# Performance work log

Measured on AMD Instinct MI355X. Metric: run time of the kernel, lower is better.

Reference implementation:

```python
import jax, jax.numpy as jnp
import numpy as np

N_NODES = 100000
N_EDGES = 1600000
N_GRAPHS = 64
IN_F = 128
H_F = 128
N_CLS = 10


def setup_inputs() -> dict:
    key = jax.random.key(0)
    ks = jax.random.split(key, 10)
    feat = jax.random.normal(ks[0], (N_NODES, IN_F), dtype=jnp.float32)
    W1 = jax.random.normal(ks[1], (IN_F, H_F), dtype=jnp.float32) * 0.05
    b1 = jax.random.normal(ks[2], (H_F,), dtype=jnp.float32) * 0.05
    W2 = jax.random.normal(ks[3], (H_F, H_F), dtype=jnp.float32) * 0.05
    b2 = jax.random.normal(ks[4], (H_F,), dtype=jnp.float32) * 0.05
    Wp = jax.random.normal(ks[5], (H_F, N_CLS), dtype=jnp.float32) * 0.05
    bp = jax.random.normal(ks[6], (N_CLS,), dtype=jnp.float32) * 0.05
    src = jax.random.randint(ks[7], (N_EDGES,), 0, N_NODES, dtype=jnp.int32)
    dst = jax.random.randint(ks[8], (N_EDGES,), 0, N_NODES, dtype=jnp.int32)
    graph_id = jnp.sort(jax.random.randint(ks[9], (N_NODES,), 0, N_GRAPHS, dtype=jnp.int32))
    return {"feat": feat, "W1": W1, "b1": b1, "W2": W2, "b2": b2,
            "Wp": Wp, "bp": bp, "src": src, "dst": dst, "graph_id": graph_id}


def reference(feat, W1, b1, W2, b2, Wp, bp, src, dst, graph_id):
    # copy_u + sum: each dst node sums features of its source neighbors
    def agg(h):
        return jax.ops.segment_sum(h[src], dst, num_segments=N_NODES)

    h = jax.nn.relu(agg(feat) @ W1 + b1)   # conv1 + ReLU
    h = jax.nn.relu(agg(h) @ W2 + b2)      # conv2 + ReLU (num_messagepasses=2)

    # dgl.mean_nodes: per-graph mean pooling over nodes
    sums = jax.ops.segment_sum(h, graph_id, num_segments=N_GRAPHS)      # [G, H]
    cnts = jax.ops.segment_sum(jnp.ones((N_NODES, 1), h.dtype), graph_id,
                               num_segments=N_GRAPHS)                    # [G, 1]
    graph_feats = sums / jnp.maximum(cnts, 1.0)
    return graph_feats @ Wp + bp
```

## Files before the change

kernel.cpp:

```cpp
#include <hip/hip_runtime.h>

#define NF 128
#define NGRAPHS 64
#define NCLS 10
#define NPARTS 64
#define PART_SHIFT 11
#define PART_NODES 2048
#define PART_CAP 36864
#define SPLIT_TILE 8192
#define AS_STRIDE 136

typedef __attribute__((ext_vector_type(8))) short bf16x8;
typedef __attribute__((ext_vector_type(4))) float f32x4;
typedef __attribute__((ext_vector_type(8))) unsigned short u16x8;

__device__ __forceinline__ float bf2f(unsigned short u) {
    union { unsigned int i; float f; } v; v.i = ((unsigned int)u) << 16; return v.f;
}
__device__ __forceinline__ unsigned short f2bf(float f) {
    union { float f; unsigned int i; } v; v.f = f;
    unsigned int lsb = (v.i >> 16) & 1;
    v.i += 0x7fffu + lsb;
    return (unsigned short)(v.i >> 16);
}

__global__ __launch_bounds__(256) void prep_all(
    const float* __restrict__ feat, unsigned short* __restrict__ featbf,
    const float* __restrict__ W1, const float* __restrict__ W2,
    unsigned short* __restrict__ Wt1, unsigned short* __restrict__ Wt2,
    float* __restrict__ sums, int* __restrict__ gcur, int nv4) {
    int i = blockIdx.x * blockDim.x + threadIdx.x;
    if (i < nv4) {
        float4 v = ((const float4*)feat)[i];
        ushort4 o;
        o.x = f2bf(v.x); o.y = f2bf(v.y); o.z = f2bf(v.z); o.w = f2bf(v.w);
        ((ushort4*)featbf)[i] = o;
    }
    if (i < 2 * NF * NF) {
        const float* W = (i < NF * NF) ? W1 : W2;
        unsigned short* Wt = (i < NF * NF) ? Wt1 : Wt2;
        int id = i & (NF * NF - 1);
        int f = id >> 7;
        int k = id & 127;
        Wt[f * NF + k] = f2bf(W[k * NF + f]);
    }
    if (i < NGRAPHS * NF) sums[i] = 0.f;
    if (i < NPARTS) gcur[i] = 0;
}

__global__ __launch_bounds__(256) void split_kernel(
    const int* __restrict__ src, const int* __restrict__ dst,
    int2* __restrict__ records, int* __restrict__ gcur, int ne) {
    __shared__ int2 stage[SPLIT_TILE];
    __shared__ int hcnt[NPARTS];
    __shared__ int hbase[NPARTS];
    __shared__ int hcur[NPARTS];
    __shared__ int hg[NPARTS];
    int t = threadIdx.x;
    int tile0 = blockIdx.x * SPLIT_TILE;
    int cnt = min(SPLIT_TILE, ne - tile0);
    if (cnt <= 0) return;
    if (t < NPARTS) hcnt[t] = 0;
    __syncthreads();
    for (int i = t; i < cnt; i += 256) {
        int d = dst[tile0 + i];
        atomicAdd(&hcnt[d >> PART_SHIFT], 1);
    }
    __syncthreads();
    if (t < NPARTS) {
        int v = hcnt[t];
        int sc = v;
        for (int off = 1; off < NPARTS; off <<= 1) {
            int u = __shfl_up(sc, off, 64);
            if (t >= off) sc += u;
        }
        hbase[t] = sc - v;
        hcur[t] = sc - v;
    }
    __syncthreads();
    for (int i = t; i < cnt; i += 256) {
        int d = dst[tile0 + i];
        int s = src[tile0 + i];
        int pos = atomicAdd(&hcur[d >> PART_SHIFT], 1);
        stage[pos] = make_int2(d, s);
    }
    if (t < NPARTS) {
        int c = hcnt[t];
        hg[t] = c ? atomicAdd(&gcur[t], c) : 0;
    }
    __syncthreads();
    for (int p = 0; p < NPARTS; ++p) {
        int c = hcnt[p];
        if (c == 0) continue;
        int b = hbase[p];
        int g = hg[p];
        if (g + c > PART_CAP) c = max(0, PART_CAP - g);
        int2* outp = records + (size_t)p * PART_CAP + g;
        for (int i = t; i < c; i += 256) outp[i] = stage[b + i];
    }
}

__global__ __launch_bounds__(64) void pscan_kernel(
    const int* __restrict__ gcur, int* __restrict__ pbase) {
    int t = threadIdx.x;
    int v = min(gcur[t], PART_CAP);
    int sc = v;
    for (int off = 1; off < NPARTS; off <<= 1) {
        int u = __shfl_up(sc, off, 64);
        if (t >= off) sc += u;
    }
    pbase[t] = sc - v;
}

__global__ __launch_bounds__(256) void build_kernel(
    const int2* __restrict__ records, const int* __restrict__ gcur,
    const int* __restrict__ pbase, int* __restrict__ offs,
    int* __restrict__ eid, int n, int ne) {
    __shared__ int deg[PART_NODES];
    __shared__ int wsum[4];
    int t = threadIdx.x;
    int p = blockIdx.x;
    int lo = p << PART_SHIFT;
    int hi = min(n, lo + PART_NODES);
    int nn = hi - lo;
    if (p == 0 && t == 0) offs[n] = ne;
    if (nn <= 0) return;

    for (int i = t; i < nn; i += 256) deg[i] = 0;
    __syncthreads();

    int L = min(gcur[p], PART_CAP);
    int base_g = pbase[p];
    const int2* rp = records + (size_t)p * PART_CAP;

    for (int i = t; i < L; i += 256) {
        int d = rp[i].x;
        atomicAdd(&deg[d - lo], 1);
    }
    __syncthreads();

    int vals[8];
    int tsum = 0;
#pragma unroll
    for (int j = 0; j < 8; ++j) {
        int idx = t * 8 + j;
        vals[j] = (idx < nn) ? deg[idx] : 0;
        tsum += vals[j];
    }
    int lane = t & 63, w = t >> 6;
    int sc = tsum;
    for (int off = 1; off < 64; off <<= 1) {
        int u = __shfl_up(sc, off, 64);
        if (lane >= off) sc += u;
    }
    if (lane == 63) wsum[w] = sc;
    __syncthreads();
    if (t == 0) {
        int a = 0;
        for (int k = 0; k < 4; ++k) { int v = wsum[k]; wsum[k] = a; a += v; }
    }
    __syncthreads();
    int run = sc - tsum + wsum[w];
#pragma unroll
    for (int j = 0; j < 8; ++j) {
        int idx = t * 8 + j;
        if (idx < nn) {
            deg[idx] = run;
            offs[lo + idx] = base_g + run;
            run += vals[j];
        }
    }
    __syncthreads();

    for (int i = t; i < L; i += 256) {
        int2 r = rp[i];
        int pos = atomicAdd(&deg[r.x - lo], 1);
        eid[base_g + pos] = r.y;
    }
}

__global__ __launch_bounds__(256) void gather_gemm1(
    const unsigned short* __restrict__ x, const int* __restrict__ offs,
    const int* __restrict__ eid, const unsigned short* __restrict__ Wt,
    const float* __restrict__ bias, unsigned short* __restrict__ out, int n) {
    __shared__ unsigned short As[16 * AS_STRIDE];
    int wave = threadIdx.x >> 6;
    int lane = threadIdx.x & 63;
    int q = lane >> 4;
    int c = lane & 15;
    int node_base = blockIdx.x * 16;

    for (int i = 0; i < 4; ++i) {
        int row = wave * 4 + i;
        int node = node_base + row;
        float acc[8] = {0.f, 0.f, 0.f, 0.f, 0.f, 0.f, 0.f, 0.f};
        if (node < n) {
            int beg = offs[node];
            int end = offs[node + 1];
            int j = beg + q;
            for (; j + 4 < end; j += 8) {
                int s0 = eid[j];
                int s1 = eid[j + 4];
                u16x8 v0 = ((const u16x8*)(x + (size_t)s0 * NF))[c];
                u16x8 v1 = ((const u16x8*)(x + (size_t)s1 * NF))[c];
#pragma unroll
                for (int r = 0; r < 8; ++r) acc[r] += bf2f(v0[r]) + bf2f(v1[r]);
            }
            if (j < end) {
                int s0 = eid[j];
                u16x8 v0 = ((const u16x8*)(x + (size_t)s0 * NF))[c];
#pragma unroll
                for (int r = 0; r < 8; ++r) acc[r] += bf2f(v0[r]);
            }
        }
#pragma unroll
        for (int r = 0; r < 8; ++r) acc[r] += __shfl_xor(acc[r], 16, 64);
#pragma unroll
        for (int r = 0; r < 8; ++r) acc[r] += __shfl_xor(acc[r], 32, 64);
        if (q == 0) {
            u16x8 o;
#pragma unroll
            for (int r = 0; r < 8; ++r) o[r] = f2bf(acc[r]);
            *(u16x8*)(&As[row * AS_STRIDE + c * 8]) = o;
        }
    }
    __syncthreads();

    int m16 = c;
    int n0 = wave * 32;
    const unsigned short* b0r = Wt + (size_t)(n0 + m16) * NF + q * 8;
    const unsigned short* b1r = b0r + 16 * NF;
    f32x4 acc0 = {0.f, 0.f, 0.f, 0.f};
    f32x4 acc1 = {0.f, 0.f, 0.f, 0.f};
#pragma unroll
    for (int kk = 0; kk < 4; ++kk) {
        bf16x8 a  = *(const bf16x8*)(&As[m16 * AS_STRIDE + kk * 32 + q * 8]);
        bf16x8 b0 = *(const bf16x8*)(b0r + kk * 32);
        bf16x8 b1 = *(const bf16x8*)(b1r + kk * 32);
        acc0 = __builtin_amdgcn_mfma_f32_16x16x32_bf16(a, b0, acc0, 0, 0, 0);
        acc1 = __builtin_amdgcn_mfma_f32_16x16x32_bf16(a, b1, acc1, 0, 0, 0);
    }
    float bias0 = bias[n0 + m16];
    float bias1 = bias[n0 + 16 + m16];
#pragma unroll
    for (int r = 0; r < 4; ++r) {
        int node = node_base + q * 4 + r;
        if (node >= n) break;
        unsigned short* o = out + (size_t)node * NF;
        o[n0 + m16]      = f2bf(fmaxf(acc0[r] + bias0, 0.f));
        o[n0 + 16 + m16] = f2bf(fmaxf(acc1[r] + bias1, 0.f));
    }
}

__global__ __launch_bounds__(256) void gather_gemm2_pool(
    const unsigned short* __restrict__ x, const int* __restrict__ offs,
    const int* __restrict__ eid, const unsigned short* __restrict__ Wt,
    const float* __restrict__ bias, const int* __restrict__ gid,
    float* __restrict__ sums, int n) {
    __shared__ unsigned short As[16 * AS_STRIDE];
    __shared__ float hblk[16][NF];
    int wave = threadIdx.x >> 6;
    int lane = threadIdx.x & 63;
    int q = lane >> 4;
    int c = lane & 15;
    int node_base = blockIdx.x * 16;

    for (int i = 0; i < 4; ++i) {
        int row = wave * 4 + i;
        int node = node_base + row;
        float acc[8] = {0.f, 0.f, 0.f, 0.f, 0.f, 0.f, 0.f, 0.f};
        if (node < n) {
            int beg = offs[node];
            int end = offs[node + 1];
            int j = beg + q;
            for (; j + 4 < end; j += 8) {
                int s0 = eid[j];
                int s1 = eid[j + 4];
                u16x8 v0 = ((const u16x8*)(x + (size_t)s0 * NF))[c];
                u16x8 v1 = ((const u16x8*)(x + (size_t)s1 * NF))[c];
#pragma unroll
                for (int r = 0; r < 8; ++r) acc[r] += bf2f(v0[r]) + bf2f(v1[r]);
            }
            if (j < end) {
                int s0 = eid[j];
                u16x8 v0 = ((const u16x8*)(x + (size_t)s0 * NF))[c];
#pragma unroll
                for (int r = 0; r < 8; ++r) acc[r] += bf2f(v0[r]);
            }
        }
#pragma unroll
        for (int r = 0; r < 8; ++r) acc[r] += __shfl_xor(acc[r], 16, 64);
#pragma unroll
        for (int r = 0; r < 8; ++r) acc[r] += __shfl_xor(acc[r], 32, 64);
        if (q == 0) {
            u16x8 o;
#pragma unroll
            for (int r = 0; r < 8; ++r) o[r] = f2bf(acc[r]);
            *(u16x8*)(&As[row * AS_STRIDE + c * 8]) = o;
        }
    }
    __syncthreads();

    int m16 = c;
    int n0 = wave * 32;
    const unsigned short* b0r = Wt + (size_t)(n0 + m16) * NF + q * 8;
    const unsigned short* b1r = b0r + 16 * NF;
    f32x4 acc0 = {0.f, 0.f, 0.f, 0.f};
    f32x4 acc1 = {0.f, 0.f, 0.f, 0.f};
#pragma unroll
    for (int kk = 0; kk < 4; ++kk) {
        bf16x8 a  = *(const bf16x8*)(&As[m16 * AS_STRIDE + kk * 32 + q * 8]);
        bf16x8 b0 = *(const bf16x8*)(b0r + kk * 32);
        bf16x8 b1 = *(const bf16x8*)(b1r + kk * 32);
        acc0 = __builtin_amdgcn_mfma_f32_16x16x32_bf16(a, b0, acc0, 0, 0, 0);
        acc1 = __builtin_amdgcn_mfma_f32_16x16x32_bf16(a, b1, acc1, 0, 0, 0);
    }
    float bias0 = bias[n0 + m16];
    float bias1 = bias[n0 + 16 + m16];
#pragma unroll
    for (int r = 0; r < 4; ++r) {
        int row = q * 4 + r;
        hblk[row][n0 + m16]      = fmaxf(acc0[r] + bias0, 0.f);
        hblk[row][n0 + 16 + m16] = fmaxf(acc1[r] + bias1, 0.f);
    }
    __syncthreads();

    int t = threadIdx.x;
    if (t < NF) {
        float acc = 0.f;
        int cur = -1;
        int lim = min(16, n - node_base);
        for (int i = 0; i < lim; ++i) {
            int g = gid[node_base + i];
            if (g != cur) {
                if (cur >= 0) atomicAdd(&sums[cur * NF + t], acc);
                acc = 0.f;
                cur = g;
            }
            acc += bf2f(f2bf(hblk[i][t]));
        }
        if (cur >= 0) atomicAdd(&sums[cur * NF + t], acc);
    }
}

__device__ __forceinline__ int lower_bound_i(const int* a, int n, int key) {
    int lo = 0, hi = n;
    while (lo < hi) {
        int mid = (lo + hi) >> 1;
        if (a[mid] < key) lo = mid + 1; else hi = mid;
    }
    return lo;
}

__global__ __launch_bounds__(64) void final_kernel(
    const float* __restrict__ sums, const int* __restrict__ gid, int n,
    const float* __restrict__ Wp, const float* __restrict__ bp,
    float* __restrict__ out) {
    __shared__ int range[2];
    int g = blockIdx.x;
    int c = threadIdx.x;
    if (c == 0) range[0] = lower_bound_i(gid, n, g);
    if (c == 1) range[1] = lower_bound_i(gid, n, g + 1);
    __syncthreads();
    if (c >= NCLS) return;
    float cnt = fmaxf((float)(range[1] - range[0]), 1.0f);
    float inv = 1.0f / cnt;
    float acc = bp[c];
#pragma unroll 8
    for (int k = 0; k < NF; ++k) {
        acc += sums[g * NF + k] * inv * Wp[k * NCLS + c];
    }
    out[g * NCLS + c] = acc;
}

extern "C" void kernel_launch(void* const* d_in, const int* in_sizes, int n_in,
                              void* d_out, int out_size, void* d_ws, size_t ws_size,
                              hipStream_t stream) {
    const float* feat = (const float*)d_in[0];
    const float* W1   = (const float*)d_in[1];
    const float* b1   = (const float*)d_in[2];
    const float* W2   = (const float*)d_in[3];
    const float* b2   = (const float*)d_in[4];
    const float* Wp   = (const float*)d_in[5];
    const float* bp   = (const float*)d_in[6];
    const int*   src  = (const int*)d_in[7];
    const int*   dst  = (const int*)d_in[8];
    const int*   gid  = (const int*)d_in[9];

    int ne = in_sizes[7];
    int n  = in_sizes[9];

    unsigned short* featbf = (unsigned short*)d_ws;
    unsigned short* h1     = featbf + (size_t)n * NF;
    int2* records = (int2*)(h1 + (size_t)n * NF);
    int* eid      = (int*)(records + (size_t)NPARTS * PART_CAP);
    float* sums   = (float*)(eid + ne);
    int* gcur     = (int*)(sums + NGRAPHS * NF);
    int* pbase    = gcur + NPARTS;
    unsigned short* Wt1 = (unsigned short*)(pbase + NPARTS);
    unsigned short* Wt2 = Wt1 + NF * NF;
    int* offs     = (int*)(Wt2 + NF * NF);

    int nv4 = n * NF / 4;
    int prepblocks = (nv4 + 255) / 256;
    int splitblocks = (ne + SPLIT_TILE - 1) / SPLIT_TILE;
    int buildblocks = (n + PART_NODES - 1) >> PART_SHIFT;
    int ggblocks = (n + 15) / 16;

    prep_all<<<prepblocks, 256, 0, stream>>>(feat, featbf, W1, W2, Wt1, Wt2,
                                             sums, gcur, nv4);
    split_kernel<<<splitblocks, 256, 0, stream>>>(src, dst, records, gcur, ne);
    pscan_kernel<<<1, 64, 0, stream>>>(gcur, pbase);
    build_kernel<<<buildblocks, 256, 0, stream>>>(records, gcur, pbase,
                                                  offs, eid, n, ne);

    gather_gemm1<<<ggblocks, 256, 0, stream>>>(featbf, offs, eid, Wt1, b1, h1, n);
    gather_gemm2_pool<<<ggblocks, 256, 0, stream>>>(h1, offs, eid, Wt2, b2, gid, sums, n);

    final_kernel<<<NGRAPHS, 64, 0, stream>>>(sums, gid, n, Wp, bp, (float*)d_out);
}
```

Baseline: 377.4 us.

## Use finer CSR partitions, fold partition scan into build, unroll gather

Raises the number of destination partitions from 64 to 256 (512 nodes each), so the CSR build runs 196 blocks instead of 49 and gets more parallelism. The separate partition-scan kernel is removed and each build block recomputes the prefix over all partition counts itself. The split kernel now copies its staged records out with 16 thread groups, one partition per group at a time, instead of looping over partitions with the whole block. The gather loops in both layers go from 2 to 4 independent row loads per iteration to raise memory-level parallelism. In exchange, every build block repeats the scan, and per-partition capacity is tighter, which could drop edges if a partition overflows.

```diff
diff --git a/kernel.cpp b/kernel.cpp
--- a/kernel.cpp
+++ b/kernel.cpp
@@ -3,10 +3,10 @@
 #define NF 128
 #define NGRAPHS 64
 #define NCLS 10
-#define NPARTS 64
-#define PART_SHIFT 11
-#define PART_NODES 2048
-#define PART_CAP 36864
+#define NPARTS 256
+#define PART_SHIFT 9
+#define PART_NODES 512
+#define PART_CAP 9216
 #define SPLIT_TILE 8192
 #define AS_STRIDE 136
 
@@ -53,30 +53,30 @@
     int2* __restrict__ records, int* __restrict__ gcur, int ne) {
     __shared__ int2 stage[SPLIT_TILE];
     __shared__ int hcnt[NPARTS];
-    __shared__ int hbase[NPARTS];
+    __shared__ int hscan[NPARTS];
     __shared__ int hcur[NPARTS];
     __shared__ int hg[NPARTS];
     int t = threadIdx.x;
     int tile0 = blockIdx.x * SPLIT_TILE;
     int cnt = min(SPLIT_TILE, ne - tile0);
     if (cnt <= 0) return;
-    if (t < NPARTS) hcnt[t] = 0;
+    hcnt[t] = 0;
     __syncthreads();
     for (int i = t; i < cnt; i += 256) {
         int d = dst[tile0 + i];
         atomicAdd(&hcnt[d >> PART_SHIFT], 1);
     }
     __syncthreads();
-    if (t < NPARTS) {
-        int v = hcnt[t];
-        int sc = v;
-        for (int off = 1; off < NPARTS; off <<= 1) {
-            int u = __shfl_up(sc, off, 64);
-            if (t >= off) sc += u;
-        }
-        hbase[t] = sc - v;
-        hcur[t] = sc - v;
-    }
+    hscan[t] = hcnt[t];
+    __syncthreads();
+    for (int off = 1; off < NPARTS; off <<= 1) {
+        int v = (t >= off) ? hscan[t - off] : 0;
+        __syncthreads();
+        hscan[t] += v;
+        __syncthreads();
+    }
+    hcur[t] = hscan[t] - hcnt[t];
+    hg[t] = hcnt[t] ? atomicAdd(&gcur[t], hcnt[t]) : 0;
     __syncthreads();
     for (int i = t; i < cnt; i += 256) {
         int d = dst[tile0 + i];
@@ -84,69 +84,56 @@
         int pos = atomicAdd(&hcur[d >> PART_SHIFT], 1);
         stage[pos] = make_int2(d, s);
     }
-    if (t < NPARTS) {
-        int c = hcnt[t];
-        hg[t] = c ? atomicAdd(&gcur[t], c) : 0;
-    }
-    __syncthreads();
-    for (int p = 0; p < NPARTS; ++p) {
+    __syncthreads();
+    int grp = t >> 4;
+    int lt = t & 15;
+    for (int p = grp; p < NPARTS; p += 16) {
         int c = hcnt[p];
         if (c == 0) continue;
-        int b = hbase[p];
+        int b = hscan[p] - c;
         int g = hg[p];
         if (g + c > PART_CAP) c = max(0, PART_CAP - g);
         int2* outp = records + (size_t)p * PART_CAP + g;
-        for (int i = t; i < c; i += 256) outp[i] = stage[b + i];
-    }
-}
-
-__global__ __launch_bounds__(64) void pscan_kernel(
-    const int* __restrict__ gcur, int* __restrict__ pbase) {
-    int t = threadIdx.x;
-    int v = min(gcur[t], PART_CAP);
-    int sc = v;
-    for (int off = 1; off < NPARTS; off <<= 1) {
-        int u = __shfl_up(sc, off, 64);
-        if (t >= off) sc += u;
-    }
-    pbase[t] = sc - v;
+        for (int i = lt; i < c; i += 16) outp[i] = stage[b + i];
+    }
 }
 
 __global__ __launch_bounds__(256) void build_kernel(
     const int2* __restrict__ records, const int* __restrict__ gcur,
-    const int* __restrict__ pbase, int* __restrict__ offs,
-    int* __restrict__ eid, int n, int ne) {
+    int* __restrict__ offs, int* __restrict__ eid, int n) {
     __shared__ int deg[PART_NODES];
+    __shared__ int ps[NPARTS];
     __shared__ int wsum[4];
     int t = threadIdx.x;
     int p = blockIdx.x;
+
+    ps[t] = min(gcur[t], PART_CAP);
+    __syncthreads();
+    for (int off = 1; off < NPARTS; off <<= 1) {
+        int v = (t >= off) ? ps[t - off] : 0;
+        __syncthreads();
+        ps[t] += v;
+        __syncthreads();
+    }
+    int L = min(gcur[p], PART_CAP);
+    int base_g = ps[p] - L;
+    if (p == 0 && t == 0) offs[n] = ps[NPARTS - 1];
+
     int lo = p << PART_SHIFT;
-    int hi = min(n, lo + PART_NODES);
-    int nn = hi - lo;
-    if (p == 0 && t == 0) offs[n] = ne;
+    int nn = min(n - lo, PART_NODES);
     if (nn <= 0) return;
 
-    for (int i = t; i < nn; i += 256) deg[i] = 0;
-    __syncthreads();
-
-    int L = min(gcur[p], PART_CAP);
-    int base_g = pbase[p];
+    deg[t] = 0;
+    deg[t + 256] = 0;
+    __syncthreads();
+
     const int2* rp = records + (size_t)p * PART_CAP;
-
-    for (int i = t; i < L; i += 256) {
-        int d = rp[i].x;
-        atomicAdd(&deg[d - lo], 1);
-    }
-    __syncthreads();
-
-    int vals[8];
-    int tsum = 0;
-#pragma unroll
-    for (int j = 0; j < 8; ++j) {
-        int idx = t * 8 + j;
-        vals[j] = (idx < nn) ? deg[idx] : 0;
-        tsum += vals[j];
-    }
+    for (int i = t; i < L; i += 256) atomicAdd(&deg[rp[i].x - lo], 1);
+    __syncthreads();
+
+    int v0 = deg[2 * t];
+    int v1 = deg[2 * t + 1];
+    int tsum = v0 + v1;
     int lane = t & 63, w = t >> 6;
     int sc = tsum;
     for (int off = 1; off < 64; off <<= 1) {
@@ -161,15 +148,11 @@
     }
     __syncthreads();
     int run = sc - tsum + wsum[w];
-#pragma unroll
-    for (int j = 0; j < 8; ++j) {
-        int idx = t * 8 + j;
-        if (idx < nn) {
-            deg[idx] = run;
-            offs[lo + idx] = base_g + run;
-            run += vals[j];
-        }
-    }
+    deg[2 * t] = run;
+    if (2 * t < nn) offs[lo + 2 * t] = base_g + run;
+    run += v0;
+    deg[2 * t + 1] = run;
+    if (2 * t + 1 < nn) offs[lo + 2 * t + 1] = base_g + run;
     __syncthreads();
 
     for (int i = t; i < L; i += 256) {
@@ -198,15 +181,20 @@
             int beg = offs[node];
             int end = offs[node + 1];
             int j = beg + q;
-            for (; j + 4 < end; j += 8) {
+            for (; j + 12 < end; j += 16) {
                 int s0 = eid[j];
                 int s1 = eid[j + 4];
+                int s2 = eid[j + 8];
+                int s3 = eid[j + 12];
                 u16x8 v0 = ((const u16x8*)(x + (size_t)s0 * NF))[c];
                 u16x8 v1 = ((const u16x8*)(x + (size_t)s1 * NF))[c];
-#pragma unroll
-                for (int r = 0; r < 8; ++r) acc[r] += bf2f(v0[r]) + bf2f(v1[r]);
+                u16x8 v2 = ((const u16x8*)(x + (size_t)s2 * NF))[c];
+                u16x8 v3 = ((const u16x8*)(x + (size_t)s3 * NF))[c];
+#pragma unroll
+                for (int r = 0; r < 8; ++r)
+                    acc[r] += (bf2f(v0[r]) + bf2f(v1[r])) + (bf2f(v2[r]) + bf2f(v3[r]));
             }
-            if (j < end) {
+            for (; j < end; j += 4) {
                 int s0 = eid[j];
                 u16x8 v0 = ((const u16x8*)(x + (size_t)s0 * NF))[c];
 #pragma unroll
@@ -273,15 +261,20 @@
             int beg = offs[node];
             int end = offs[node + 1];
             int j = beg + q;
-            for (; j + 4 < end; j += 8) {
+            for (; j + 12 < end; j += 16) {
                 int s0 = eid[j];
                 int s1 = eid[j + 4];
+                int s2 = eid[j + 8];
+                int s3 = eid[j + 12];
                 u16x8 v0 = ((const u16x8*)(x + (size_t)s0 * NF))[c];
                 u16x8 v1 = ((const u16x8*)(x + (size_t)s1 * NF))[c];
-#pragma unroll
-                for (int r = 0; r < 8; ++r) acc[r] += bf2f(v0[r]) + bf2f(v1[r]);
+                u16x8 v2 = ((const u16x8*)(x + (size_t)s2 * NF))[c];
+                u16x8 v3 = ((const u16x8*)(x + (size_t)s3 * NF))[c];
+#pragma unroll
+                for (int r = 0; r < 8; ++r)
+                    acc[r] += (bf2f(v0[r]) + bf2f(v1[r])) + (bf2f(v2[r]) + bf2f(v3[r]));
             }
-            if (j < end) {
+            for (; j < end; j += 4) {
                 int s0 = eid[j];
                 u16x8 v0 = ((const u16x8*)(x + (size_t)s0 * NF))[c];
 #pragma unroll
@@ -396,8 +389,7 @@
     int* eid      = (int*)(records + (size_t)NPARTS * PART_CAP);
     float* sums   = (float*)(eid + ne);
     int* gcur     = (int*)(sums + NGRAPHS * NF);
-    int* pbase    = gcur + NPARTS;
-    unsigned short* Wt1 = (unsigned short*)(pbase + NPARTS);
+    unsigned short* Wt1 = (unsigned short*)(gcur + NPARTS);
     unsigned short* Wt2 = Wt1 + NF * NF;
     int* offs     = (int*)(Wt2 + NF * NF);
 
@@ -410,9 +402,7 @@
     prep_all<<<prepblocks, 256, 0, stream>>>(feat, featbf, W1, W2, Wt1, Wt2,
                                              sums, gcur, nv4);
     split_kernel<<<splitblocks, 256, 0, stream>>>(src, dst, records, gcur, ne);
-    pscan_kernel<<<1, 64, 0, stream>>>(gcur, pbase);
-    build_kernel<<<buildblocks, 256, 0, stream>>>(records, gcur, pbase,
-                                                  offs, eid, n, ne);
+    build_kernel<<<buildblocks, 256, 0, stream>>>(records, gcur, offs, eid, n);
 
     gather_gemm1<<<ggblocks, 256, 0, stream>>>(featbf, offs, eid, Wt1, b1, h1, n);
     gather_gemm2_pool<<<ggblocks, 256, 0, stream>>>(h1, offs, eid, Wt2, b2, gid, sums, n);
```

After: 330.2 us. 1.14x faster.
